# Performance work log

Measured on AMD Instinct MI355X. Metric: run time of the kernel, lower is better.

The kernel has to match this reference:

```python
import jax, jax.numpy as jnp
import numpy as np

H, DK, OUT = 8, 32, 256
SQRT_DK = float(np.sqrt(DK))


def _proj(feat, W, b):
    # (N, in) -> (N, H, DK)
    return (feat @ W + b).reshape(feat.shape[0], H, DK)


def _rel(k_src, v_src, q_dst, src, dst, att_w, msg_w, pri, n_dst):
    # HGT-style per-relation edge attention + segment softmax + aggregation.
    key = jnp.einsum('ehd,hdk->ehk', k_src[src], att_w)          # (E,H,DK)
    att = (q_dst[dst] * key).sum(-1) * pri / SQRT_DK             # (E,H)
    val = jnp.einsum('ehd,hdk->ehk', v_src[src], msg_w)          # (E,H,DK)
    m = jax.ops.segment_max(att, dst, num_segments=n_dst)
    m = jnp.where(jnp.isfinite(m), m, 0.0)
    e = jnp.exp(att - m[dst])
    s = jax.ops.segment_sum(e, dst, num_segments=n_dst)
    alpha = e / jnp.maximum(s[dst], 1e-9)
    h = jax.ops.segment_sum(alpha[..., None] * val, dst, num_segments=n_dst)
    return jax.nn.relu(h.reshape(n_dst, OUT))                    # relu per etype (reduce_func)


def _ln(x, g, b):
    mu = x.mean(-1, keepdims=True)
    var = ((x - mu) ** 2).mean(-1, keepdims=True)
    return (x - mu) / jnp.sqrt(var + 1e-5) * g + b


def _forward(feat_word, feat_topic, feat_doc, Wk, bk, Wq, bq, Wv, bv, Wa, ba,
             ln_scale, ln_bias, skip, rel_pri, rel_att, rel_msg,
             src_ww, dst_ww, src_wt, dst_wt, src_wd, dst_wd,
             src_tt, dst_tt, src_td, dst_td):
    # ntype order: word=0, topic=1, doc=2; etype order: ww=0, wt=1, wd=2, tt=3, td=4
    Nw, Nt, Nd = feat_word.shape[0], feat_topic.shape[0], feat_doc.shape[0]
    k_w, q_w, v_w = _proj(feat_word, Wk[0], bk[0]), _proj(feat_word, Wq[0], bq[0]), _proj(feat_word, Wv[0], bv[0])
    k_t, q_t, v_t = _proj(feat_topic, Wk[1], bk[1]), _proj(feat_topic, Wq[1], bq[1]), _proj(feat_topic, Wv[1], bv[1])
    q_d = _proj(feat_doc, Wq[2], bq[2])
    t_ww = _rel(k_w, v_w, q_w, src_ww, dst_ww, rel_att[0], rel_msg[0], rel_pri[0], Nw)
    t_wt = _rel(k_w, v_w, q_t, src_wt, dst_wt, rel_att[1], rel_msg[1], rel_pri[1], Nt)
    t_wd = _rel(k_w, v_w, q_d, src_wd, dst_wd, rel_att[2], rel_msg[2], rel_pri[2], Nd)
    t_tt = _rel(k_t, v_t, q_t, src_tt, dst_tt, rel_att[3], rel_msg[3], rel_pri[3], Nt)
    t_td = _rel(k_t, v_t, q_d, src_td, dst_td, rel_att[4], rel_msg[4], rel_pri[4], Nd)
    # cross_reducer='mean' across etypes targeting each ntype
    t_word, t_topic, t_doc = t_ww, (t_wt + t_tt) * 0.5, (t_wd + t_td) * 0.5
    outs = []
    for i, (t, feat) in enumerate([(t_word, feat_word), (t_topic, feat_topic), (t_doc, feat_doc)]):
        a = jax.nn.sigmoid(skip[i])
        trans = (t @ Wa[i] + ba[i]) * a + feat * (1.0 - a)
        outs.append(_ln(trans, ln_scale[i], ln_bias[i]))
    return jnp.concatenate(outs, axis=0)  # (Nw+Nt+Nd, OUT)


def setup_inputs() -> dict:
    key = jax.random.key(0)
    ks = jax.random.split(key, 32)
    Nw, Nt, Nd, D = 20000, 2000, 5000, 256
    E = {'ww': (150000, Nw, Nw), 'wt': (80000, Nw, Nt), 'wd': (80000, Nw, Nd),
         'tt': (20000, Nt, Nt), 'td': (40000, Nt, Nd)}
    inp = {
        'feat_word': jax.random.normal(ks[0], (Nw, D), jnp.float32),
        'feat_topic': jax.random.normal(ks[1], (Nt, D), jnp.float32),
        'feat_doc': jax.random.normal(ks[2], (Nd, D), jnp.float32),
        'Wk': jax.random.normal(ks[3], (3, D, D), jnp.float32) * 0.05,
        'bk': jax.random.normal(ks[4], (3, D), jnp.float32) * 0.02,
        'Wq': jax.random.normal(ks[5], (3, D, D), jnp.float32) * 0.05,
        'bq': jax.random.normal(ks[6], (3, D), jnp.float32) * 0.02,
        'Wv': jax.random.normal(ks[7], (3, D, D), jnp.float32) * 0.05,
        'bv': jax.random.normal(ks[8], (3, D), jnp.float32) * 0.02,
        'Wa': jax.random.normal(ks[9], (3, D, D), jnp.float32) * 0.05,
        'ba': jax.random.normal(ks[10], (3, D), jnp.float32) * 0.02,
        'ln_scale': jnp.ones((3, D), jnp.float32),
        'ln_bias': jnp.zeros((3, D), jnp.float32),
        'skip': jnp.ones((3,), jnp.float32),
        'rel_pri': jnp.ones((5, H), jnp.float32),
        'rel_att': jax.random.normal(ks[11], (5, H, DK, DK), jnp.float32) * 0.1,
        'rel_msg': jax.random.normal(ks[12], (5, H, DK, DK), jnp.float32) * 0.1,
    }
    for i, (et, (ne, ns, nd)) in enumerate(E.items()):
        inp['src_' + et] = jax.random.randint(ks[13 + 2 * i], (ne,), 0, ns, jnp.int32)
        inp['dst_' + et] = jax.random.randint(ks[14 + 2 * i], (ne,), 0, nd, jnp.int32)
    return inp


def reference(feat_word, feat_topic, feat_doc, Wk, bk, Wq, bq, Wv, bv, Wa, ba,
              ln_scale, ln_bias, skip, rel_pri, rel_att, rel_msg,
              src_ww, dst_ww, src_wt, dst_wt, src_wd, dst_wd,
              src_tt, dst_tt, src_td, dst_td):
    return _forward(feat_word, feat_topic, feat_doc, Wk, bk, Wq, bq, Wv, bv, Wa, ba,
                    ln_scale, ln_bias, skip, rel_pri, rel_att, rel_msg,
                    src_ww, dst_ww, src_wt, dst_wt, src_wd, dst_wd,
                    src_tt, dst_tt, src_td, dst_td)
```

## Files before the change

kernel.cpp:

```cpp
#include <hip/hip_runtime.h>

static constexpr int NW = 20000, NT = 2000, ND = 5000;
static constexpr int E_WW = 150000, E_WT = 80000, E_WD = 80000, E_TT = 20000, E_TD = 40000;

typedef short bf16x8 __attribute__((ext_vector_type(8)));
typedef float f32x4 __attribute__((ext_vector_type(4)));
typedef float f32x2 __attribute__((ext_vector_type(2)));

__device__ __forceinline__ unsigned short f2bf(float f) {
  union { float f; unsigned int u; } c; c.f = f;
  unsigned int u = c.u;
  u += 0x7fffu + ((u >> 16) & 1u);
  return (unsigned short)(u >> 16);
}
__device__ __forceinline__ float bf2f(unsigned short h) {
  union { unsigned int u; float f; } c; c.u = ((unsigned int)h) << 16; return c.f;
}
__device__ __forceinline__ bf16x8 pack8(float4 a, float4 b) {
  bf16x8 r;
  r[0] = (short)f2bf(a.x); r[1] = (short)f2bf(a.y); r[2] = (short)f2bf(a.z); r[3] = (short)f2bf(a.w);
  r[4] = (short)f2bf(b.x); r[5] = (short)f2bf(b.y); r[6] = (short)f2bf(b.z); r[7] = (short)f2bf(b.w);
  return r;
}
__device__ __forceinline__ unsigned char f2fp8(float x) {
  int p = __builtin_amdgcn_cvt_pk_fp8_f32(x, x, 0, false);
  return (unsigned char)(p & 0xff);
}

struct CsrDesc {
  const int* dst[5];
  const int* src[5];
  int E[5], N[5], cbase[5];
};

struct PrepArgs {
  const float* psrc[7]; unsigned short* pdst[7];
  const float* wq[5]; const float* bqp[5];
  unsigned short* qdst[5];
  float* beff;
  const float* att;
  const float* msg; unsigned short* wvp;
  CsrDesc dsc;
  int* counts;
  int bEff, bHw, bHist, bTot;
};
__global__ __launch_bounds__(256) void prep_kernel(PrepArgs a) {
  __shared__ float tile[32][33];
  int b = blockIdx.x;
  int tid = threadIdx.x;
  if (b < a.bEff) {
    int m = b >> 6, bk = ((b >> 3) & 7) * 32, bn = (b & 7) * 32;
    const float* W = a.psrc[m];
    unsigned short* WT = a.pdst[m];
    int tx = tid & 31, ty = tid >> 5;
#pragma unroll
    for (int i = 0; i < 32; i += 8)
      tile[ty + i][tx] = W[(size_t)(bk + ty + i) * 256 + bn + tx];
    __syncthreads();
#pragma unroll
    for (int i = 0; i < 32; i += 8)
      WT[(size_t)(bn + ty + i) * 256 + bk + tx] = f2bf(tile[tx][ty + i]);
  } else if (b < a.bHw) {
    int t = (b - a.bEff) * 256 + tid;
    if (t < 5 * 65536) {
      int r = t >> 16, rem = t & 65535;
      int n = rem >> 8, kk = rem & 255;
      int h = n >> 5, j = n & 31;
      const float* wrow = a.wq[r] + kk * 256 + h * 32;
      const float* arow = a.att + r * 8192 + h * 1024 + j * 32;
      float s = 0.f;
#pragma unroll
      for (int d = 0; d < 32; d += 4) {
        float4 wv = *(const float4*)(wrow + d);
        float4 av = *(const float4*)(arow + d);
        s += wv.x * av.x + wv.y * av.y + wv.z * av.z + wv.w * av.w;
      }
      a.qdst[r][n * 256 + kk] = f2bf(s);
    } else {
      int idx = t - 5 * 65536;
      if (idx < 1280) {
        int r = idx >> 8, n = idx & 255;
        int h = n >> 5, j = n & 31;
        const float* brow = a.bqp[r] + h * 32;
        const float* arow = a.att + r * 8192 + h * 1024 + j * 32;
        float s = 0.f;
#pragma unroll
        for (int d = 0; d < 32; d += 4) {
          float4 bv = *(const float4*)(brow + d);
          float4 av = *(const float4*)(arow + d);
          s += bv.x * av.x + bv.y * av.y + bv.z * av.z + bv.w * av.w;
        }
        a.beff[r * 256 + n] = s;
      }
    }
  } else if (b < a.bHist) {
    int t = (b - a.bHw) * 256 + tid;
    if (t < 5 * 8192) {
      int m = t >> 13, rem = t & 8191;
      int hc = rem >> 9, idx = rem & 511;
      int lane = idx >> 3, j = idx & 7;
      int h = hc >> 1, c = hc & 1;
      int k = (lane >> 4) * 8 + j, n = c * 16 + (lane & 15);
      a.wvp[t] = f2bf(a.msg[(size_t)m * 8192 + h * 1024 + k * 32 + n]);
    }
  } else {
    int t = (b - a.bHist) * 256 + tid;
    int r = 0, base = 0;
    while (r < 5 && t >= base + a.dsc.E[r]) { base += a.dsc.E[r]; r++; }
    if (r >= 5) return;
    int e = t - base;
    atomicAdd(a.counts + a.dsc.cbase[r] + a.dsc.dst[r][e], 1);
  }
}

struct ProjAll {
  const float* A[3];
  const unsigned short* WT[3];
  const float* bias[3][4];
  unsigned char* outB[3][4];
  int esz[3][4];
  int M[3], ncolg[3], bcum[4];
  const int* counts; int* offsets; int scanN;
};
__global__ __launch_bounds__(256) void proj_all(ProjAll pa) {
  __shared__ unsigned short As[64 * 256];
  __shared__ unsigned short Bs[256 * 64];
  __shared__ int wpart2[4];
  __shared__ int carry2;
  const int tid = threadIdx.x;
  if ((int)blockIdx.x >= pa.bcum[3]) {
    int lane = tid & 63, w = tid >> 6;
    if (tid == 0) carry2 = 0;
    __syncthreads();
    const int N = pa.scanN;
    for (int base = 0; base < N; base += 1024) {
      int idx = base + tid * 4;
      int v0 = 0, v1 = 0, v2 = 0, v3 = 0;
      if (idx + 3 < N) {
        int4 t4 = *(const int4*)(pa.counts + idx);
        v0 = t4.x; v1 = t4.y; v2 = t4.z; v3 = t4.w;
      } else if (idx < N) {
        v0 = pa.counts[idx];
        if (idx + 1 < N) v1 = pa.counts[idx + 1];
        if (idx + 2 < N) v2 = pa.counts[idx + 2];
      }
      int ts = v0 + v1 + v2 + v3;
      int x = ts;
#pragma unroll
      for (int d = 1; d < 64; d <<= 1) {
        int t = __shfl_up(x, d, 64);
        if (lane >= d) x += t;
      }
      if (lane == 63) wpart2[w] = x;
      __syncthreads();
      if (tid == 0) {
        int s = 0;
#pragma unroll
        for (int j = 0; j < 4; j++) { int t = wpart2[j]; wpart2[j] = s; s += t; }
      }
      __syncthreads();
      int excl = carry2 + wpart2[w] + (x - ts);
      if (idx < N)     pa.offsets[idx]     = excl;
      if (idx + 1 < N) pa.offsets[idx + 1] = excl + v0;
      if (idx + 2 < N) pa.offsets[idx + 2] = excl + v0 + v1;
      if (idx + 3 < N) pa.offsets[idx + 3] = excl + v0 + v1 + v2;
      __syncthreads();
      if (tid == 255) carry2 = excl + ts;
      __syncthreads();
    }
    if (tid == 0) pa.offsets[N] = carry2;
    return;
  }
  int nt = 0;
  while (nt < 2 && (int)blockIdx.x >= pa.bcum[nt + 1]) nt++;
  const int bm = (blockIdx.x - pa.bcum[nt]) * 64;
  const float* A = pa.A[nt];
  const unsigned short* WT = pa.WT[nt];
  const int M = pa.M[nt];
  const int wave = tid >> 6, lane = tid & 63;
  const int ar = wave * 16 + (lane & 15);
  const int swz = lane & 7;
#pragma unroll
  for (int i = 0; i < 8; i++) {
    int c = i * 256 + tid;
    int row = c >> 5, sv = c & 31;
    int srow = bm + row;
    float4 a0 = make_float4(0.f, 0.f, 0.f, 0.f), a1 = a0;
    if (srow < M) {
      a0 = *(const float4*)(A + (size_t)srow * 256 + sv * 8);
      a1 = *(const float4*)(A + (size_t)srow * 256 + sv * 8 + 4);
    }
    *(bf16x8*)&As[row * 256 + ((sv ^ (row & 7)) * 8)] = pack8(a0, a1);
  }
  const int ncolg = pa.ncolg[nt];
  for (int cg = 0; cg < ncolg; cg++) {
    f32x4 acc[16] = {};
    for (int k0 = 0; k0 < 256; k0 += 64) {
      __syncthreads();
#pragma unroll
      for (int i = 0; i < 8; i++) {
        int c = tid + i * 256;
        int row = c >> 3, sl = c & 7;
        bf16x8 bv = *(const bf16x8*)(WT + (size_t)(cg * 256 + row) * 256 + k0 + sl * 8);
        *(bf16x8*)&Bs[row * 64 + ((sl ^ (row & 7)) * 8)] = bv;
      }
      __syncthreads();
#pragma unroll
      for (int kk = 0; kk < 2; kk++) {
        int slot = kk * 4 + (lane >> 4);
        int gslot = (k0 >> 3) + slot;
        bf16x8 av = *(const bf16x8*)&As[ar * 256 + ((gslot ^ swz) * 8)];
#pragma unroll
        for (int nf = 0; nf < 16; nf++) {
          int br = nf * 16 + (lane & 15);
          bf16x8 bv = *(const bf16x8*)&Bs[br * 64 + ((slot ^ swz) * 8)];
          acc[nf] = __builtin_amdgcn_mfma_f32_16x16x32_bf16(av, bv, acc[nf], 0, 0, 0);
        }
      }
    }
    const int col = lane & 15;
    const float* bias = pa.bias[nt][cg];
    unsigned char* outB = pa.outB[nt][cg];
    const int esz = pa.esz[nt][cg];
#pragma unroll
    for (int nf = 0; nf < 16; nf++) {
      float bsv = bias[nf * 16 + col];
      int idx = nf * 16 + col;
#pragma unroll
      for (int rr = 0; rr < 4; rr++) {
        int row = bm + wave * 16 + (lane >> 4) * 4 + rr;
        if (row < M) {
          float v = acc[nf][rr] + bsv;
          if (esz == 2) *(unsigned short*)(outB + (size_t)row * 512 + idx * 2) = f2bf(v);
          else          outB[(size_t)row * 512 + idx] = f2fp8(v);
        }
      }
    }
  }
}

__global__ void scatter5(CsrDesc d, const int* __restrict__ offsets, int* __restrict__ cursor,
                         int* __restrict__ ssrc) {
  int t = blockIdx.x * blockDim.x + threadIdx.x;
  int r = 0, base = 0;
  while (r < 5 && t >= base + d.E[r]) { base += d.E[r]; r++; }
  if (r >= 5) return;
  int e = t - base;
  int dn = d.dst[r][e];
  int pos = offsets[d.cbase[r] + dn] + atomicAdd(cursor + d.cbase[r] + dn, 1);
  ssrc[pos] = d.src[r][e];
}

struct AttArgs {
  const unsigned short* qh[5]; const unsigned char* kv8[5];
  const int* offs[5]; unsigned short* agg[5];
  const int* ssrc;
  const float* pri;
  int bcum[6]; int Ndst[5];
};
__global__ __launch_bounds__(256) void fused_att_agg(AttArgs a) {
  int r = 0;
  while (r < 4 && (int)blockIdx.x >= a.bcum[r + 1]) r++;
  int wave = threadIdx.x >> 6, lane = threadIdx.x & 63;
  int node = (blockIdx.x - a.bcum[r]) * 4 + wave;
  if (node >= a.Ndst[r]) return;
  const unsigned short* qh = a.qh[r];
  const unsigned char* kvb = a.kv8[r];
  const int* ssrc = a.ssrc;
  const int* offs = a.offs[r];
  int h = lane >> 3;
  float prih = a.pri[r * 8 + h] * 0.17677669529663687f;
  int r0 = offs[node], r1 = offs[node + 1];
  float4 acc = make_float4(0.f, 0.f, 0.f, 0.f);
  if (r0 < r1) {
    ushort4 qv = *(const ushort4*)(qh + (size_t)node * 256 + lane * 4);
    float q0 = bf2f(qv.x), q1 = bf2f(qv.y), q2 = bf2f(qv.z), q3 = bf2f(qv.w);
    float m = -1e30f, s = 0.f;
    for (int i = r0; i < r1; i += 2) {
      int sA = ssrc[i];
      bool two = (i + 1 < r1);
      int sB = two ? ssrc[i + 1] : sA;
      const unsigned char* pA = kvb + (size_t)sA * 512 + lane * 4;
      const unsigned char* pB = kvb + (size_t)sB * 512 + lane * 4;
      unsigned int kuA = *(const unsigned int*)pA;
      unsigned int kuB = *(const unsigned int*)pB;
      unsigned int vuA = *(const unsigned int*)(pA + 256);
      unsigned int vuB = *(const unsigned int*)(pB + 256);
      f32x2 ka01 = __builtin_amdgcn_cvt_pk_f32_fp8((int)kuA, false);
      f32x2 ka23 = __builtin_amdgcn_cvt_pk_f32_fp8((int)kuA, true);
      f32x2 kb01 = __builtin_amdgcn_cvt_pk_f32_fp8((int)kuB, false);
      f32x2 kb23 = __builtin_amdgcn_cvt_pk_f32_fp8((int)kuB, true);
      float dA = q0 * ka01[0] + q1 * ka01[1] + q2 * ka23[0] + q3 * ka23[1];
      float dB = q0 * kb01[0] + q1 * kb01[1] + q2 * kb23[0] + q3 * kb23[1];
      dA += __shfl_xor(dA, 1, 64); dB += __shfl_xor(dB, 1, 64);
      dA += __shfl_xor(dA, 2, 64); dB += __shfl_xor(dB, 2, 64);
      dA += __shfl_xor(dA, 4, 64); dB += __shfl_xor(dB, 4, 64);
      float lA = dA * prih;
      float lB = two ? dB * prih : -1e30f;
      float mn = fmaxf(m, fmaxf(lA, lB));
      float sc = __expf(m - mn);
      float wA = __expf(lA - mn);
      float wB = __expf(lB - mn);
      m = mn;
      s = s * sc + wA + wB;
      f32x2 va01 = __builtin_amdgcn_cvt_pk_f32_fp8((int)vuA, false);
      f32x2 va23 = __builtin_amdgcn_cvt_pk_f32_fp8((int)vuA, true);
      f32x2 vb01 = __builtin_amdgcn_cvt_pk_f32_fp8((int)vuB, false);
      f32x2 vb23 = __builtin_amdgcn_cvt_pk_f32_fp8((int)vuB, true);
      acc.x = acc.x * sc + wA * va01[0] + wB * vb01[0];
      acc.y = acc.y * sc + wA * va01[1] + wB * vb01[1];
      acc.z = acc.z * sc + wA * va23[0] + wB * vb23[0];
      acc.w = acc.w * sc + wA * va23[1] + wB * vb23[1];
    }
    float inv = 1.f / fmaxf(s, 1e-9f);
    acc.x *= inv; acc.y *= inv; acc.z *= inv; acc.w *= inv;
  }
  ushort4 o;
  o.x = f2bf(acc.x); o.y = f2bf(acc.y); o.z = f2bf(acc.z); o.w = f2bf(acc.w);
  *(ushort4*)(a.agg[r] + (size_t)node * 256 + lane * 4) = o;
}

struct MsgArgs {
  const unsigned short* aggA[3]; const unsigned short* aggB[3];
  const unsigned short* fA[3]; const unsigned short* fB[3];
  unsigned short* t[3];
  float scale[3];
  int N[3]; int bcum[4];
};
__global__ __launch_bounds__(256) void msg_transform_all(MsgArgs a) {
  int g = 0;
  while (g < 2 && (int)blockIdx.x >= a.bcum[g + 1]) g++;
  int local = blockIdx.x - a.bcum[g];
  const unsigned short* aggA = a.aggA[g];
  const unsigned short* aggB = a.aggB[g];
  const unsigned short* fA = a.fA[g];
  const unsigned short* fB = a.fB[g];
  unsigned short* t = a.t[g];
  float scale = a.scale[g];
  int N = a.N[g];
  int wave = threadIdx.x >> 6, lane = threadIdx.x & 63;
  int r0 = local * 64 + wave * 16;
  int arow = r0 + (lane & 15);
  bool valid = arow < N;
  int kofs = (lane >> 4) * 8;
  f32x4 z{};
#pragma unroll
  for (int h = 0; h < 8; h++) {
    bf16x8 aA{}, aB{};
    if (valid) {
      aA = *(const bf16x8*)(aggA + (size_t)arow * 256 + h * 32 + kofs);
      if (aggB) aB = *(const bf16x8*)(aggB + (size_t)arow * 256 + h * 32 + kofs);
    }
#pragma unroll
    for (int c = 0; c < 2; c++) {
      bf16x8 bA = *(const bf16x8*)(fA + ((h * 2 + c) * 64 + lane) * 8);
      f32x4 oA = __builtin_amdgcn_mfma_f32_16x16x32_bf16(aA, bA, z, 0, 0, 0);
      f32x4 oB = z;
      if (aggB) {
        bf16x8 bB = *(const bf16x8*)(fB + ((h * 2 + c) * 64 + lane) * 8);
        oB = __builtin_amdgcn_mfma_f32_16x16x32_bf16(aB, bB, z, 0, 0, 0);
      }
      int colc = h * 32 + c * 16 + (lane & 15);
#pragma unroll
      for (int rr = 0; rr < 4; rr++) {
        int row = r0 + (lane >> 4) * 4 + rr;
        if (row < N) {
          float v = fmaxf(oA[rr], 0.f) + fmaxf(oB[rr], 0.f);
          t[(size_t)row * 256 + colc] = f2bf(v * scale);
        }
      }
    }
  }
}

struct OutAll {
  const unsigned short* tA[3]; const unsigned short* WT[3];
  const float* ba[3]; const float* feat[3];
  const float* gamma[3]; const float* beta[3];
  float* op[3];
  int M[3], bcum[4];
  const float* skipv;
};
__global__ __launch_bounds__(256) void out_all_ln(OutAll oa) {
  __shared__ unsigned short As[64 * 64];
  __shared__ unsigned short Bs[256 * 64];
  int g = 0;
  while (g < 2 && (int)blockIdx.x >= oa.bcum[g + 1]) g++;
  const int bm = (blockIdx.x - oa.bcum[g]) * 64;
  const unsigned short* tA = oa.tA[g];
  const unsigned short* WT = oa.WT[g];
  const int M = oa.M[g];
  const int tid = threadIdx.x, wave = tid >> 6, lane = tid & 63;
  f32x4 acc[16] = {};
  const int ar = wave * 16 + (lane & 15);
  const int swz = lane & 7;
  for (int k0 = 0; k0 < 256; k0 += 64) {
#pragma unroll
    for (int i = 0; i < 2; i++) {
      int c = tid + i * 256;
      int row = c >> 3, sl = c & 7;
      int srow = bm + row;
      bf16x8 av{};
      if (srow < M) av = *(const bf16x8*)(tA + (size_t)srow * 256 + k0 + sl * 8);
      *(bf16x8*)&As[row * 64 + (sl ^ (row & 7)) * 8] = av;
    }
#pragma unroll
    for (int i = 0; i < 8; i++) {
      int c = tid + i * 256;
      int row = c >> 3, sl = c & 7;
      bf16x8 bv = *(const bf16x8*)(WT + (size_t)row * 256 + k0 + sl * 8);
      *(bf16x8*)&Bs[row * 64 + (sl ^ (row & 7)) * 8] = bv;
    }
    __syncthreads();
#pragma unroll
    for (int kk = 0; kk < 2; kk++) {
      int slot = kk * 4 + (lane >> 4);
      bf16x8 av = *(const bf16x8*)&As[ar * 64 + ((slot ^ swz) * 8)];
#pragma unroll
      for (int nf = 0; nf < 16; nf++) {
        int br = nf * 16 + (lane & 15);
        bf16x8 bv = *(const bf16x8*)&Bs[br * 64 + ((slot ^ swz) * 8)];
        acc[nf] = __builtin_amdgcn_mfma_f32_16x16x32_bf16(av, bv, acc[nf], 0, 0, 0);
      }
    }
    __syncthreads();
  }
  const int c16 = lane & 15;
  float a_skip = 1.f / (1.f + __expf(-oa.skipv[g]));
  float one_m = 1.f - a_skip;
  const float* gamma = oa.gamma[g];
  const float* beta = oa.beta[g];
  const float* ba = oa.ba[g];
  const float* feat = oa.feat[g];
  float* outp = oa.op[g];
  float gg[16], bb[16], bia[16];
#pragma unroll
  for (int nf = 0; nf < 16; nf++) {
    gg[nf] = gamma[nf * 16 + c16];
    bb[nf] = beta[nf * 16 + c16];
    bia[nf] = ba[nf * 16 + c16];
  }
#pragma unroll
  for (int rr = 0; rr < 4; rr++) {
    int row = bm + wave * 16 + (lane >> 4) * 4 + rr;
    bool valid = row < M;
#pragma unroll
    for (int nf = 0; nf < 16; nf++) {
      float fv = valid ? feat[(size_t)row * 256 + nf * 16 + c16] : 0.f;
      acc[nf][rr] = (acc[nf][rr] + bia[nf]) * a_skip + fv * one_m;
    }
    float p = 0.f;
#pragma unroll
    for (int nf = 0; nf < 16; nf++) p += acc[nf][rr];
    p += __shfl_xor(p, 1, 16); p += __shfl_xor(p, 2, 16);
    p += __shfl_xor(p, 4, 16); p += __shfl_xor(p, 8, 16);
    float mu = p * (1.f / 256.f);
    float qv = 0.f;
#pragma unroll
    for (int nf = 0; nf < 16; nf++) { float dd = acc[nf][rr] - mu; qv += dd * dd; }
    qv += __shfl_xor(qv, 1, 16); qv += __shfl_xor(qv, 2, 16);
    qv += __shfl_xor(qv, 4, 16); qv += __shfl_xor(qv, 8, 16);
    float rstd = rsqrtf(qv * (1.f / 256.f) + 1e-5f);
    if (valid) {
#pragma unroll
      for (int nf = 0; nf < 16; nf++)
        outp[(size_t)row * 256 + nf * 16 + c16] = (acc[nf][rr] - mu) * rstd * gg[nf] + bb[nf];
    }
  }
}

extern "C" void kernel_launch(void* const* d_in, const int* in_sizes, int n_in,
                              void* d_out, int out_size, void* d_ws, size_t ws_size,
                              hipStream_t stream) {
  const float* feat_w = (const float*)d_in[0];
  const float* feat_t = (const float*)d_in[1];
  const float* feat_d = (const float*)d_in[2];
  const float* Wk = (const float*)d_in[3];
  const float* bk = (const float*)d_in[4];
  const float* Wq = (const float*)d_in[5];
  const float* bq = (const float*)d_in[6];
  const float* Wv = (const float*)d_in[7];
  const float* bv = (const float*)d_in[8];
  const float* Wa = (const float*)d_in[9];
  const float* ba = (const float*)d_in[10];
  const float* ln_scale = (const float*)d_in[11];
  const float* ln_bias = (const float*)d_in[12];
  const float* skip = (const float*)d_in[13];
  const float* rel_pri = (const float*)d_in[14];
  const float* rel_att = (const float*)d_in[15];
  const float* rel_msg = (const float*)d_in[16];
  const int* src_ww = (const int*)d_in[17];
  const int* dst_ww = (const int*)d_in[18];
  const int* src_wt = (const int*)d_in[19];
  const int* dst_wt = (const int*)d_in[20];
  const int* src_wd = (const int*)d_in[21];
  const int* dst_wd = (const int*)d_in[22];
  const int* src_tt = (const int*)d_in[23];
  const int* dst_tt = (const int*)d_in[24];
  const int* src_td = (const int*)d_in[25];
  const int* dst_td = (const int*)d_in[26];
  float* out = (float*)d_out;
  float* ws = (float*)d_ws;

  size_t off = 0;
  auto allocF = [&](size_t nf) { float* p = ws + off; off += nf; return p; };
  unsigned char* kv_w = (unsigned char*)allocF(2560000);
  unsigned char* kv_t = (unsigned char*)allocF(256000);
  unsigned short* qhat0 = (unsigned short*)allocF(2560000);
  unsigned short* qhat1 = (unsigned short*)allocF(256000);
  unsigned short* qhat2 = (unsigned short*)allocF(640000);
  unsigned short* qhat3 = (unsigned short*)allocF(256000);
  unsigned short* qhat4 = (unsigned short*)allocF(640000);
  unsigned short* aggr0 = (unsigned short*)allocF(2560000);
  unsigned short* aggr1 = (unsigned short*)allocF(256000);
  unsigned short* aggr2 = (unsigned short*)allocF(640000);
  unsigned short* aggr3 = (unsigned short*)allocF(256000);
  unsigned short* aggr4 = (unsigned short*)allocF(640000);
  unsigned short* t_word  = (unsigned short*)allocF(2560000);
  unsigned short* t_topic = (unsigned short*)allocF(256000);
  unsigned short* t_doc   = (unsigned short*)allocF(640000);
  unsigned short* WTw = (unsigned short*)allocF(98304);
  unsigned short* WTt = (unsigned short*)allocF(131072);
  unsigned short* WTd = (unsigned short*)allocF(65536);
  unsigned short* WTa = (unsigned short*)allocF(98304);
  unsigned short* wvp = (unsigned short*)allocF(20480);
  float* bq_eff = allocF(1280);
  int* counts  = (int*)allocF(34000);
  int* cursor  = (int*)allocF(34000);
  int* offsets = (int*)allocF(34004);
  int* ssrc    = (int*)allocF(370000);

  dim3 b256(256);
  auto cdiv = [](int a, int b) { return (a + b - 1) / b; };

  CsrDesc dsc;
  dsc.dst[0] = dst_ww; dsc.dst[1] = dst_wt; dsc.dst[2] = dst_wd; dsc.dst[3] = dst_tt; dsc.dst[4] = dst_td;
  dsc.src[0] = src_ww; dsc.src[1] = src_wt; dsc.src[2] = src_wd; dsc.src[3] = src_tt; dsc.src[4] = src_td;
  int Es[5] = {E_WW, E_WT, E_WD, E_TT, E_TD};
  int Ns[5] = {NW, NT, ND, NT, ND};
  int cb = 0;
  for (int r = 0; r < 5; r++) {
    dsc.E[r] = Es[r]; dsc.N[r] = Ns[r]; dsc.cbase[r] = cb;
    cb += Ns[r];
  }

  hipMemsetAsync(counts, 0, (size_t)68000 * sizeof(int), stream);

  {
    PrepArgs pr;
    pr.psrc[0] = Wk;           pr.pdst[0] = WTw + 65536;
    pr.psrc[1] = Wv;           pr.pdst[1] = WTw + 131072;
    pr.psrc[2] = Wk + 65536;   pr.pdst[2] = WTt;
    pr.psrc[3] = Wv + 65536;   pr.pdst[3] = WTt + 65536;
    pr.psrc[4] = Wa;           pr.pdst[4] = WTa;
    pr.psrc[5] = Wa + 65536;   pr.pdst[5] = WTa + 65536;
    pr.psrc[6] = Wa + 131072;  pr.pdst[6] = WTa + 131072;
    pr.wq[0] = Wq;           pr.bqp[0] = bq;        pr.qdst[0] = WTw;
    pr.wq[1] = Wq + 65536;   pr.bqp[1] = bq + 256;  pr.qdst[1] = WTt + 131072;
    pr.wq[2] = Wq + 131072;  pr.bqp[2] = bq + 512;  pr.qdst[2] = WTd;
    pr.wq[3] = Wq + 65536;   pr.bqp[3] = bq + 256;  pr.qdst[3] = WTt + 196608;
    pr.wq[4] = Wq + 131072;  pr.bqp[4] = bq + 512;  pr.qdst[4] = WTd + 65536;
    pr.beff = bq_eff;
    pr.att = rel_att;
    pr.msg = rel_msg; pr.wvp = wvp;
    pr.dsc = dsc; pr.counts = counts;
    int nPack = 7 * 64;
    int nEff  = cdiv(5 * 65536 + 1280, 256);
    int nHw   = cdiv(5 * 8192, 256);
    int nHist = cdiv(370000, 256);
    pr.bEff  = nPack;
    pr.bHw   = nPack + nEff;
    pr.bHist = nPack + nEff + nHw;
    pr.bTot  = nPack + nEff + nHw + nHist;
    prep_kernel<<<pr.bTot, b256, 0, stream>>>(pr);
  }

  {
    ProjAll pa;
    pa.A[0] = feat_w; pa.A[1] = feat_t; pa.A[2] = feat_d;
    pa.WT[0] = WTw;   pa.WT[1] = WTt;   pa.WT[2] = WTd;
    pa.M[0] = NW; pa.M[1] = NT; pa.M[2] = ND;
    pa.bias[0][0] = bq_eff;       pa.outB[0][0] = (unsigned char*)qhat0; pa.esz[0][0] = 2;
    pa.bias[0][1] = bk;           pa.outB[0][1] = kv_w;                  pa.esz[0][1] = 1;
    pa.bias[0][2] = bv;           pa.outB[0][2] = kv_w + 256;            pa.esz[0][2] = 1;
    pa.bias[0][3] = bq_eff;       pa.outB[0][3] = (unsigned char*)qhat0; pa.esz[0][3] = 2;
    pa.bias[1][0] = bk + 256;     pa.outB[1][0] = kv_t;                  pa.esz[1][0] = 1;
    pa.bias[1][1] = bv + 256;     pa.outB[1][1] = kv_t + 256;            pa.esz[1][1] = 1;
    pa.bias[1][2] = bq_eff + 256; pa.outB[1][2] = (unsigned char*)qhat1; pa.esz[1][2] = 2;
    pa.bias[1][3] = bq_eff + 768; pa.outB[1][3] = (unsigned char*)qhat3; pa.esz[1][3] = 2;
    pa.bias[2][0] = bq_eff + 512;  pa.outB[2][0] = (unsigned char*)qhat2; pa.esz[2][0] = 2;
    pa.bias[2][1] = bq_eff + 1024; pa.outB[2][1] = (unsigned char*)qhat4; pa.esz[2][1] = 2;
    pa.bias[2][2] = bq_eff;        pa.outB[2][2] = (unsigned char*)qhat2; pa.esz[2][2] = 2;
    pa.bias[2][3] = bq_eff;        pa.outB[2][3] = (unsigned char*)qhat2; pa.esz[2][3] = 2;
    pa.ncolg[0] = 3; pa.ncolg[1] = 4; pa.ncolg[2] = 2;
    int nb0 = cdiv(NW, 64), nb1 = cdiv(NT, 64), nb2 = cdiv(ND, 64);
    pa.bcum[0] = 0; pa.bcum[1] = nb0; pa.bcum[2] = nb0 + nb1; pa.bcum[3] = nb0 + nb1 + nb2;
    pa.counts = counts; pa.offsets = offsets; pa.scanN = 34000;
    proj_all<<<pa.bcum[3] + 1, b256, 0, stream>>>(pa);
  }

  scatter5<<<cdiv(370000, 256), b256, 0, stream>>>(dsc, offsets, cursor, ssrc);

  int NdstA[5] = {NW, NT, ND, NT, ND};

  {
    AttArgs aa;
    aa.qh[0] = qhat0; aa.qh[1] = qhat1; aa.qh[2] = qhat2; aa.qh[3] = qhat3; aa.qh[4] = qhat4;
    aa.kv8[0] = aa.kv8[1] = aa.kv8[2] = kv_w; aa.kv8[3] = aa.kv8[4] = kv_t;
    unsigned short* aggs[5] = {aggr0, aggr1, aggr2, aggr3, aggr4};
    aa.ssrc = ssrc;
    int bc = 0;
    for (int r = 0; r < 5; r++) {
      aa.offs[r] = offsets + dsc.cbase[r];
      aa.agg[r] = aggs[r];
      aa.Ndst[r] = NdstA[r];
      aa.bcum[r] = bc; bc += cdiv(NdstA[r], 4);
    }
    aa.bcum[5] = bc;
    aa.pri = rel_pri;
    fused_att_agg<<<bc, b256, 0, stream>>>(aa);
  }

  {
    MsgArgs ma;
    ma.aggA[0] = aggr0; ma.aggB[0] = nullptr;
    ma.fA[0] = wvp;             ma.fB[0] = wvp;
    ma.t[0] = t_word;  ma.scale[0] = 1.0f;  ma.N[0] = NW;
    ma.aggA[1] = aggr1; ma.aggB[1] = aggr3;
    ma.fA[1] = wvp + 8192;      ma.fB[1] = wvp + 3 * 8192;
    ma.t[1] = t_topic; ma.scale[1] = 0.5f;  ma.N[1] = NT;
    ma.aggA[2] = aggr2; ma.aggB[2] = aggr4;
    ma.fA[2] = wvp + 2 * 8192;  ma.fB[2] = wvp + 4 * 8192;
    ma.t[2] = t_doc;   ma.scale[2] = 0.5f;  ma.N[2] = ND;
    int bc = 0;
    for (int g = 0; g < 3; g++) { ma.bcum[g] = bc; bc += cdiv(ma.N[g], 64); }
    ma.bcum[3] = bc;
    msg_transform_all<<<bc, b256, 0, stream>>>(ma);
  }

  {
    OutAll oa;
    oa.tA[0] = t_word;  oa.tA[1] = t_topic; oa.tA[2] = t_doc;
    oa.WT[0] = WTa; oa.WT[1] = WTa + 65536; oa.WT[2] = WTa + 131072;
    oa.ba[0] = ba; oa.ba[1] = ba + 256; oa.ba[2] = ba + 512;
    oa.feat[0] = feat_w; oa.feat[1] = feat_t; oa.feat[2] = feat_d;
    oa.gamma[0] = ln_scale; oa.gamma[1] = ln_scale + 256; oa.gamma[2] = ln_scale + 512;
    oa.beta[0] = ln_bias; oa.beta[1] = ln_bias + 256; oa.beta[2] = ln_bias + 512;
    oa.op[0] = out; oa.op[1] = out + (size_t)NW * 256; oa.op[2] = out + (size_t)(NW + NT) * 256;
    oa.M[0] = NW; oa.M[1] = NT; oa.M[2] = ND;
    int bc = 0;
    for (int g = 0; g < 3; g++) { oa.bcum[g] = bc; bc += cdiv(oa.M[g], 64); }
    oa.bcum[3] = bc;
    oa.skipv = skip;
    out_all_ln<<<bc, b256, 0, stream>>>(oa);
  }

  (void)in_sizes; (void)n_in; (void)out_size; (void)ws_size;
}
```

Baseline: 209.2 us.

## Drop LDS staging in projection and output GEMMs, split column groups across blocks

Both dense GEMM kernels stop staging A and B tiles in shared memory. Each lane now loads its MFMA fragments straight from global memory, with the small weight matrices expected to stay cache-resident. The projection kernel also launches one block per (row tile, column group) pair instead of looping over column groups inside a block. This raises parallelism and removes LDS traffic and barriers. The cost is that the fp32 A rows are reloaded and reconverted once per column group, and the direct fragment loads are less coalesced.

```diff
diff --git a/kernel.cpp b/kernel.cpp
--- a/kernel.cpp
+++ b/kernel.cpp
@@ -123,8 +123,6 @@
   const int* counts; int* offsets; int scanN;
 };
 __global__ __launch_bounds__(256) void proj_all(ProjAll pa) {
-  __shared__ unsigned short As[64 * 256];
-  __shared__ unsigned short Bs[256 * 64];
   __shared__ int wpart2[4];
   __shared__ int carry2;
   const int tid = threadIdx.x;
@@ -173,67 +171,49 @@
   }
   int nt = 0;
   while (nt < 2 && (int)blockIdx.x >= pa.bcum[nt + 1]) nt++;
-  const int bm = (blockIdx.x - pa.bcum[nt]) * 64;
+  int local = blockIdx.x - pa.bcum[nt];
+  const int ncolg = pa.ncolg[nt];
+  const int rt = local / ncolg, cg = local % ncolg;
   const float* A = pa.A[nt];
   const unsigned short* WT = pa.WT[nt];
   const int M = pa.M[nt];
   const int wave = tid >> 6, lane = tid & 63;
-  const int ar = wave * 16 + (lane & 15);
-  const int swz = lane & 7;
-#pragma unroll
-  for (int i = 0; i < 8; i++) {
-    int c = i * 256 + tid;
-    int row = c >> 5, sv = c & 31;
-    int srow = bm + row;
-    float4 a0 = make_float4(0.f, 0.f, 0.f, 0.f), a1 = a0;
-    if (srow < M) {
-      a0 = *(const float4*)(A + (size_t)srow * 256 + sv * 8);
-      a1 = *(const float4*)(A + (size_t)srow * 256 + sv * 8 + 4);
-    }
-    *(bf16x8*)&As[row * 256 + ((sv ^ (row & 7)) * 8)] = pack8(a0, a1);
-  }
-  const int ncolg = pa.ncolg[nt];
-  for (int cg = 0; cg < ncolg; cg++) {
-    f32x4 acc[16] = {};
-    for (int k0 = 0; k0 < 256; k0 += 64) {
-      __syncthreads();
-#pragma unroll
-      for (int i = 0; i < 8; i++) {
-        int c = tid + i * 256;
-        int row = c >> 3, sl = c & 7;
-        bf16x8 bv = *(const bf16x8*)(WT + (size_t)(cg * 256 + row) * 256 + k0 + sl * 8);
-        *(bf16x8*)&Bs[row * 64 + ((sl ^ (row & 7)) * 8)] = bv;
-      }
-      __syncthreads();
-#pragma unroll
-      for (int kk = 0; kk < 2; kk++) {
-        int slot = kk * 4 + (lane >> 4);
-        int gslot = (k0 >> 3) + slot;
-        bf16x8 av = *(const bf16x8*)&As[ar * 256 + ((gslot ^ swz) * 8)];
-#pragma unroll
-        for (int nf = 0; nf < 16; nf++) {
-          int br = nf * 16 + (lane & 15);
-          bf16x8 bv = *(const bf16x8*)&Bs[br * 64 + ((slot ^ swz) * 8)];
-          acc[nf] = __builtin_amdgcn_mfma_f32_16x16x32_bf16(av, bv, acc[nf], 0, 0, 0);
-        }
-      }
-    }
-    const int col = lane & 15;
-    const float* bias = pa.bias[nt][cg];
-    unsigned char* outB = pa.outB[nt][cg];
-    const int esz = pa.esz[nt][cg];
+  const int bm = rt * 64;
+  const int arow = bm + wave * 16 + (lane & 15);
+  const bool valid = arow < M;
+  const int kofs = (lane >> 4) * 8;
+  const float* Aptr = A + (size_t)arow * 256 + kofs;
+  const unsigned short* Bptr = WT + (size_t)(cg * 256 + (lane & 15)) * 256 + kofs;
+  f32x4 acc[16] = {};
+#pragma unroll
+  for (int kk = 0; kk < 8; kk++) {
+    bf16x8 af{};
+    if (valid) {
+      float4 a0 = *(const float4*)(Aptr + kk * 32);
+      float4 a1 = *(const float4*)(Aptr + kk * 32 + 4);
+      af = pack8(a0, a1);
+    }
 #pragma unroll
     for (int nf = 0; nf < 16; nf++) {
-      float bsv = bias[nf * 16 + col];
-      int idx = nf * 16 + col;
-#pragma unroll
-      for (int rr = 0; rr < 4; rr++) {
-        int row = bm + wave * 16 + (lane >> 4) * 4 + rr;
-        if (row < M) {
-          float v = acc[nf][rr] + bsv;
-          if (esz == 2) *(unsigned short*)(outB + (size_t)row * 512 + idx * 2) = f2bf(v);
-          else          outB[(size_t)row * 512 + idx] = f2fp8(v);
-        }
+      bf16x8 bf_ = *(const bf16x8*)(Bptr + (size_t)nf * 4096 + kk * 32);
+      acc[nf] = __builtin_amdgcn_mfma_f32_16x16x32_bf16(af, bf_, acc[nf], 0, 0, 0);
+    }
+  }
+  const int col = lane & 15;
+  const float* bias = pa.bias[nt][cg];
+  unsigned char* outB = pa.outB[nt][cg];
+  const int esz = pa.esz[nt][cg];
+#pragma unroll
+  for (int nf = 0; nf < 16; nf++) {
+    float bsv = bias[nf * 16 + col];
+    int idx = nf * 16 + col;
+#pragma unroll
+    for (int rr = 0; rr < 4; rr++) {
+      int row = bm + wave * 16 + (lane >> 4) * 4 + rr;
+      if (row < M) {
+        float v = acc[nf][rr] + bsv;
+        if (esz == 2) *(unsigned short*)(outB + (size_t)row * 512 + idx * 2) = f2bf(v);
+        else          outB[(size_t)row * 512 + idx] = f2fp8(v);
       }
     }
   }
@@ -382,8 +362,6 @@
   const float* skipv;
 };
 __global__ __launch_bounds__(256) void out_all_ln(OutAll oa) {
-  __shared__ unsigned short As[64 * 64];
-  __shared__ unsigned short Bs[256 * 64];
   int g = 0;
   while (g < 2 && (int)blockIdx.x >= oa.bcum[g + 1]) g++;
   const int bm = (blockIdx.x - oa.bcum[g]) * 64;
@@ -391,39 +369,21 @@
   const unsigned short* WT = oa.WT[g];
   const int M = oa.M[g];
   const int tid = threadIdx.x, wave = tid >> 6, lane = tid & 63;
+  const int arow = bm + wave * 16 + (lane & 15);
+  const bool valid_a = arow < M;
+  const int kofs = (lane >> 4) * 8;
+  const unsigned short* Aptr = tA + (size_t)arow * 256 + kofs;
+  const unsigned short* Bptr = WT + (size_t)(lane & 15) * 256 + kofs;
   f32x4 acc[16] = {};
-  const int ar = wave * 16 + (lane & 15);
-  const int swz = lane & 7;
-  for (int k0 = 0; k0 < 256; k0 += 64) {
-#pragma unroll
-    for (int i = 0; i < 2; i++) {
-      int c = tid + i * 256;
-      int row = c >> 3, sl = c & 7;
-      int srow = bm + row;
-      bf16x8 av{};
-      if (srow < M) av = *(const bf16x8*)(tA + (size_t)srow * 256 + k0 + sl * 8);
-      *(bf16x8*)&As[row * 64 + (sl ^ (row & 7)) * 8] = av;
-    }
-#pragma unroll
-    for (int i = 0; i < 8; i++) {
-      int c = tid + i * 256;
-      int row = c >> 3, sl = c & 7;
-      bf16x8 bv = *(const bf16x8*)(WT + (size_t)row * 256 + k0 + sl * 8);
-      *(bf16x8*)&Bs[row * 64 + (sl ^ (row & 7)) * 8] = bv;
-    }
-    __syncthreads();
-#pragma unroll
-    for (int kk = 0; kk < 2; kk++) {
-      int slot = kk * 4 + (lane >> 4);
-      bf16x8 av = *(const bf16x8*)&As[ar * 64 + ((slot ^ swz) * 8)];
-#pragma unroll
-      for (int nf = 0; nf < 16; nf++) {
-        int br = nf * 16 + (lane & 15);
-        bf16x8 bv = *(const bf16x8*)&Bs[br * 64 + ((slot ^ swz) * 8)];
-        acc[nf] = __builtin_amdgcn_mfma_f32_16x16x32_bf16(av, bv, acc[nf], 0, 0, 0);
-      }
-    }
-    __syncthreads();
+#pragma unroll
+  for (int kk = 0; kk < 8; kk++) {
+    bf16x8 af{};
+    if (valid_a) af = *(const bf16x8*)(Aptr + kk * 32);
+#pragma unroll
+    for (int nf = 0; nf < 16; nf++) {
+      bf16x8 bf_ = *(const bf16x8*)(Bptr + (size_t)nf * 4096 + kk * 32);
+      acc[nf] = __builtin_amdgcn_mfma_f32_16x16x32_bf16(af, bf_, acc[nf], 0, 0, 0);
+    }
   }
   const int c16 = lane & 15;
   float a_skip = 1.f / (1.f + __expf(-oa.skipv[g]));
@@ -593,7 +553,7 @@
     pa.bias[2][2] = bq_eff;        pa.outB[2][2] = (unsigned char*)qhat2; pa.esz[2][2] = 2;
     pa.bias[2][3] = bq_eff;        pa.outB[2][3] = (unsigned char*)qhat2; pa.esz[2][3] = 2;
     pa.ncolg[0] = 3; pa.ncolg[1] = 4; pa.ncolg[2] = 2;
-    int nb0 = cdiv(NW, 64), nb1 = cdiv(NT, 64), nb2 = cdiv(ND, 64);
+    int nb0 = cdiv(NW, 64) * 3, nb1 = cdiv(NT, 64) * 4, nb2 = cdiv(ND, 64) * 2;
     pa.bcum[0] = 0; pa.bcum[1] = nb0; pa.bcum[2] = nb0 + nb1; pa.bcum[3] = nb0 + nb1 + nb2;
     pa.counts = counts; pa.offsets = offsets; pa.scanN = 34000;
     proj_all<<<pa.bcum[3] + 1, b256, 0, stream>>>(pa);
```

New measurement: 273.3 us. +30.6%, slower.
